# Optimization experiments

Measured on AMD Instinct MI355X. Metric: run time of the kernel, lower is better.

## Reference

```python
import jax, jax.numpy as jnp
import numpy as np

EPS = 1e-6
H, HKV, D = 32, 8, 64          # heads, kv heads, head_dim
E, TOP_K, FF = 8, 2, 1024      # experts, top-k, expert intermediate
HID = 2048


def rms_norm(x, w):
    xf = x.astype(jnp.float32)
    var = jnp.mean(xf * xf, axis=-1, keepdims=True)
    return (w * (xf * jax.lax.rsqrt(var + EPS)).astype(x.dtype))


def rotate_half(x):
    x1, x2 = jnp.split(x, 2, axis=-1)
    return jnp.concatenate([-x2, x1], axis=-1)


def apply_rope(q, k, cos, sin):
    # cos/sin: [B,S,rd] -> [B,1,S,rd]
    cos = cos[:, None, :, :]
    sin = sin[:, None, :, :]
    rd = cos.shape[-1]
    q_rot, q_pass = q[..., :rd], q[..., rd:]
    k_rot, k_pass = k[..., :rd], k[..., rd:]
    q_emb = q_rot * cos + rotate_half(q_rot) * sin
    k_emb = k_rot * cos + rotate_half(k_rot) * sin
    return (jnp.concatenate([q_emb, q_pass], -1), jnp.concatenate([k_emb, k_pass], -1))


def attention(x, cos, sin, wq, wk, wv, wo):
    B, S, _ = x.shape
    q = (x @ wq).reshape(B, S, H, D).transpose(0, 2, 1, 3)      # [B,H,S,D]
    k = (x @ wk).reshape(B, S, HKV, D).transpose(0, 2, 1, 3)    # [B,Hk,S,D]
    v = (x @ wv).reshape(B, S, HKV, D).transpose(0, 2, 1, 3)
    q, k = apply_rope(q, k, cos, sin)
    rep = H // HKV
    k = jnp.repeat(k, rep, axis=1)
    v = jnp.repeat(v, rep, axis=1)
    scale = D ** -0.5
    scores = jnp.einsum('bhqd,bhkd->bhqk', q, k) * scale
    causal = jnp.triu(jnp.full((S, S), -jnp.inf, dtype=scores.dtype), k=1)
    scores = scores + causal
    probs = jax.nn.softmax(scores.astype(jnp.float32), axis=-1).astype(q.dtype)
    out = jnp.einsum('bhqk,bhkd->bhqd', probs, v)
    out = out.transpose(0, 2, 1, 3).reshape(B, S, H * D)
    return out @ wo


def moe(x, gate_w, corr_bias, w1, w2, w3):
    B, S, Dm = x.shape
    xf = x.reshape(-1, Dm)                                      # [T, Dm]
    T = xf.shape[0]
    logits = xf @ gate_w                                        # [T, E]
    rw = jax.nn.sigmoid(logits.astype(jnp.float32))
    scores = rw + corr_bias
    _, sel = jax.lax.top_k(scores, TOP_K)                       # [T, k]
    tw = jnp.take_along_axis(rw, sel, axis=-1)
    tw = tw / jnp.sum(tw, axis=-1, keepdims=True)
    # dense [T, E] combine weights (zero for unselected experts)
    cw = jnp.zeros((T, E), dtype=xf.dtype).at[jnp.arange(T)[:, None], sel].set(tw.astype(xf.dtype))
    # run every expert densely, combine with sparse weights (same math as gather/scatter loop)
    h = jax.nn.silu(jnp.einsum('td,edf->etf', xf, w1)) * jnp.einsum('td,edf->etf', xf, w3)
    eo = jnp.einsum('etf,efd->etd', h, w2)                      # [E, T, Dm]
    out = jnp.einsum('etd,te->td', eo, cw)
    return out.reshape(B, S, Dm)


def setup_inputs() -> dict:
    key = jax.random.key(0)
    ks = jax.random.split(key, 16)
    s = 0.02
    return {
        'hidden_states': jax.random.normal(ks[0], (2, 1024, HID), jnp.float32),
        'cos': jax.random.uniform(ks[1], (2, 1024, D), jnp.float32),
        'sin': jax.random.uniform(ks[2], (2, 1024, D), jnp.float32),
        'ln1_w': jnp.ones((HID,), jnp.float32),
        'ln2_w': jnp.ones((HID,), jnp.float32),
        'wq': jax.random.normal(ks[3], (HID, H * D), jnp.float32) * s,
        'wk': jax.random.normal(ks[4], (HID, HKV * D), jnp.float32) * s,
        'wv': jax.random.normal(ks[5], (HID, HKV * D), jnp.float32) * s,
        'wo': jax.random.normal(ks[6], (H * D, HID), jnp.float32) * s,
        'gate_w': jax.random.normal(ks[7], (HID, E), jnp.float32) * s,
        'corr_bias': jnp.zeros((E,), jnp.float32),
        'w1': jax.random.normal(ks[8], (E, HID, FF), jnp.float32) * s,
        'w2': jax.random.normal(ks[9], (E, FF, HID), jnp.float32) * s,
        'w3': jax.random.normal(ks[10], (E, HID, FF), jnp.float32) * s,
    }


def reference(hidden_states, cos, sin, ln1_w, ln2_w, wq, wk, wv, wo, gate_w, corr_bias, w1, w2, w3):
    residual = hidden_states
    h = rms_norm(hidden_states, ln1_w)
    h = attention(h, cos, sin, wq, wk, wv, wo)
    h = residual + h
    residual = h
    h = rms_norm(h, ln2_w)
    h = moe(h, gate_w, corr_bias, w1, w2, w3)
    return residual + h
```

## Files before the change

### kernel.cpp

```cpp
#include <hip/hip_runtime.h>
#include <hip/hip_bf16.h>

#define DEV static __device__ __forceinline__

typedef __attribute__((ext_vector_type(8))) short short8;
typedef __attribute__((ext_vector_type(8))) __bf16 bf16x8;
typedef __attribute__((ext_vector_type(4))) float floatx4;

DEV short f2bf(float f) {
  unsigned u = __builtin_bit_cast(unsigned, f);
  unsigned r = (u + 0x7fffu + ((u >> 16) & 1u)) >> 16;
  return (short)(unsigned short)r;
}
DEV float bf2f(short s) {
  unsigned u = ((unsigned)(unsigned short)s) << 16;
  return __builtin_bit_cast(float, u);
}
DEV floatx4 mfma16(short8 a, short8 b, floatx4 c) {
  return __builtin_amdgcn_mfma_f32_16x16x32_bf16(
      __builtin_bit_cast(bf16x8, a), __builtin_bit_cast(bf16x8, b), c, 0, 0, 0);
}

#define VMCNT(n) asm volatile("s_waitcnt vmcnt(" #n ")" ::: "memory")
#define SBAR() __builtin_amdgcn_s_barrier()

DEV int sw2(int r) { return (r ^ (r >> 2)) & 3; }

DEV const short* sbase(const short* src, int ld, int row0, int id) {
  int r = id >> 2, cc = id & 3;
  return src + (long)(row0 + r) * ld + ((cc ^ sw2(r)) << 3);
}
DEV void sissue(short* ldsbuf, const short* base, int k0, int tid, int slotbase) {
  int wave = tid >> 6;
  __builtin_amdgcn_global_load_lds(
      (const __attribute__((address_space(1))) void*)(base + k0),
      (__attribute__((address_space(3))) void*)(ldsbuf + (slotbase + wave * 64) * 8),
      16, 0, 0);
}
DEV short8 rdfrag(const short* lds, int row, int l4) {
  return *(const short8*)(lds + row * 32 + ((l4 ^ sw2(row)) << 3));
}

DEV const short* sb64(const short* src, int ld, int row0, int id) {
  int r = id >> 3, c = id & 7;
  return src + (long)(row0 + r) * ld + ((c ^ (r & 7)) << 3);
}
DEV const short* sb64g(const short* src, int ld, const int* rows, int p0, int plim,
                       int id) {
  int r = id >> 3, c = id & 7;
  int pi = p0 + r;
  if (pi > plim) pi = plim;
  return src + (long)rows[pi] * ld + ((c ^ (r & 7)) << 3);
}
DEV short8 rd64(const short* lds, int row, int ch) {
  return *(const short8*)(lds + row * 64 + ((ch ^ (row & 7)) << 3));
}

__global__ __launch_bounds__(256) void k_gemm_qkv(
    const short* Ah, const short* Al, const short* Bh, const short* Bl,
    short* qbh, short* qbl, short* kbh, short* kbl, short* vbh, short* vbl,
    const float* cs, const float* sn) {
  const int K = 2048;
  __shared__ __align__(16) short AsH[2][4096], AsL[2][4096], BsH[2][4096], BsL[2][4096];
  int tid = threadIdx.x, lane = tid & 63, wave = tid >> 6;
  int l15 = lane & 15, l4 = lane >> 4;
  int wm = wave >> 1, wn = wave & 1;
  int bid = blockIdx.y * 24 + blockIdx.x;
  int swz = (bid & 7) * 48 + (bid >> 3);
  int bx = swz % 24, by = swz / 24;
  int m0 = by * 128, n0 = bx * 128;

  const short* bAH0 = sbase(Ah, K, m0, tid);
  const short* bAH1 = sbase(Ah, K, m0, tid + 256);
  const short* bAL0 = sbase(Al, K, m0, tid);
  const short* bAL1 = sbase(Al, K, m0, tid + 256);
  const short* bBH0 = sbase(Bh, K, n0, tid);
  const short* bBH1 = sbase(Bh, K, n0, tid + 256);
  const short* bBL0 = sbase(Bl, K, n0, tid);
  const short* bBL1 = sbase(Bl, K, n0, tid + 256);

  auto STAGE = [&](int buf, int k0) {
    sissue(AsH[buf], bAH0, k0, tid, 0);
    sissue(AsH[buf], bAH1, k0, tid, 256);
    sissue(AsL[buf], bAL0, k0, tid, 0);
    sissue(AsL[buf], bAL1, k0, tid, 256);
    sissue(BsH[buf], bBH0, k0, tid, 0);
    sissue(BsH[buf], bBH1, k0, tid, 256);
    sissue(BsL[buf], bBL0, k0, tid, 0);
    sissue(BsL[buf], bBL1, k0, tid, 256);
  };

  floatx4 zero4 = {0.f, 0.f, 0.f, 0.f};
  floatx4 acc[4][4];
#pragma unroll
  for (int i = 0; i < 4; ++i)
#pragma unroll
    for (int j = 0; j < 4; ++j) acc[i][j] = zero4;

  STAGE(0, 0);
  STAGE(1, 32);
  int cur = 0;
  for (int k0 = 0; k0 < K; k0 += 32) {
    if (k0 + 64 < K) VMCNT(8); else VMCNT(0);
    SBAR();
    short8 ah[4], al[4], bh2[4], bl2[4];
#pragma unroll
    for (int mi = 0; mi < 4; ++mi) {
      ah[mi] = rdfrag(AsH[cur], wm * 64 + mi * 16 + l15, l4);
      al[mi] = rdfrag(AsL[cur], wm * 64 + mi * 16 + l15, l4);
    }
#pragma unroll
    for (int nt = 0; nt < 4; ++nt) {
      bh2[nt] = rdfrag(BsH[cur], wn * 64 + nt * 16 + l15, l4);
      bl2[nt] = rdfrag(BsL[cur], wn * 64 + nt * 16 + l15, l4);
    }
#pragma unroll
    for (int mi = 0; mi < 4; ++mi)
#pragma unroll
      for (int nt = 0; nt < 4; ++nt) {
        acc[mi][nt] = mfma16(al[mi], bh2[nt], acc[mi][nt]);
        acc[mi][nt] = mfma16(ah[mi], bl2[nt], acc[mi][nt]);
        acc[mi][nt] = mfma16(ah[mi], bh2[nt], acc[mi][nt]);
      }
    SBAR();
    if (k0 + 64 < K) STAGE(cur, k0 + 64);
    cur ^= 1;
  }

  int hb = n0 + wn * 64;
  bool isq = hb < 2048, isk = (!isq) && hb < 2560;
  if (isq || isk) {
#pragma unroll
    for (int mi = 0; mi < 4; ++mi)
#pragma unroll
      for (int ntp = 0; ntp < 2; ++ntp)
#pragma unroll
        for (int j = 0; j < 4; ++j) {
          int row = m0 + wm * 64 + mi * 16 + l4 * 4 + j;
          int d = ntp * 16 + l15;
          float x0 = acc[mi][ntp][j], x1 = acc[mi][ntp + 2][j];
          float c0 = cs[row * 64 + d], c1 = cs[row * 64 + d + 32];
          float s0 = sn[row * 64 + d], s1 = sn[row * 64 + d + 32];
          float y0 = x0 * c0 - x1 * s0;
          float y1 = x1 * c1 + x0 * s1;
          if (isq) { y0 *= 0.125f; y1 *= 0.125f; }
          acc[mi][ntp][j] = y0;
          acc[mi][ntp + 2][j] = y1;
        }
  }
  short* Ch; short* Cl; int ldc, coff;
  if (isq)      { Ch = qbh; Cl = qbl; ldc = 2048; coff = hb; }
  else if (isk) { Ch = kbh; Cl = kbl; ldc = 512;  coff = hb - 2048; }
  else          { Ch = vbh; Cl = vbl; ldc = 512;  coff = hb - 2560; }
#pragma unroll
  for (int mi = 0; mi < 4; ++mi)
#pragma unroll
    for (int nt = 0; nt < 4; ++nt) {
      int row = m0 + wm * 64 + mi * 16 + l4 * 4;
      int col = coff + nt * 16 + l15;
#pragma unroll
      for (int j = 0; j < 4; ++j) {
        float v = acc[mi][nt][j];
        long ix = (long)(row + j) * ldc + col;
        short hi = f2bf(v);
        Ch[ix] = hi;
        Cl[ix] = f2bf(v - bf2f(hi));
      }
    }
}

__global__ __launch_bounds__(256) void k_gemm_wo(const short* Ah, const short* Al,
                                                 const short* Bh, const short* Bl,
                                                 const float* resid, float* out) {
  const int K = 2048;
  __shared__ __align__(16) short AsH[2][4096], AsL[2][4096], BsH[2][2048], BsL[2][2048];
  int tid = threadIdx.x, lane = tid & 63, wave = tid >> 6;
  int l15 = lane & 15, l4 = lane >> 4;
  int m0 = blockIdx.y * 128, n0 = blockIdx.x * 64;

  const short* bAH0 = sbase(Ah, K, m0, tid);
  const short* bAH1 = sbase(Ah, K, m0, tid + 256);
  const short* bAL0 = sbase(Al, K, m0, tid);
  const short* bAL1 = sbase(Al, K, m0, tid + 256);
  const short* bBH0 = sbase(Bh, K, n0, tid);
  const short* bBL0 = sbase(Bl, K, n0, tid);

  auto STAGE = [&](int buf, int k0) {
    sissue(AsH[buf], bAH0, k0, tid, 0);
    sissue(AsH[buf], bAH1, k0, tid, 256);
    sissue(AsL[buf], bAL0, k0, tid, 0);
    sissue(AsL[buf], bAL1, k0, tid, 256);
    sissue(BsH[buf], bBH0, k0, tid, 0);
    sissue(BsL[buf], bBL0, k0, tid, 0);
  };

  floatx4 zero4 = {0.f, 0.f, 0.f, 0.f};
  floatx4 acc[2][4];
#pragma unroll
  for (int i = 0; i < 2; ++i)
#pragma unroll
    for (int j = 0; j < 4; ++j) acc[i][j] = zero4;

  STAGE(0, 0);
  STAGE(1, 32);
  int cur = 0;
  for (int k0 = 0; k0 < K; k0 += 32) {
    if (k0 + 64 < K) VMCNT(6); else VMCNT(0);
    SBAR();
    short8 ah[2], al[2], bh2[4], bl2[4];
#pragma unroll
    for (int mi = 0; mi < 2; ++mi) {
      ah[mi] = rdfrag(AsH[cur], wave * 32 + mi * 16 + l15, l4);
      al[mi] = rdfrag(AsL[cur], wave * 32 + mi * 16 + l15, l4);
    }
#pragma unroll
    for (int nt = 0; nt < 4; ++nt) {
      bh2[nt] = rdfrag(BsH[cur], nt * 16 + l15, l4);
      bl2[nt] = rdfrag(BsL[cur], nt * 16 + l15, l4);
    }
#pragma unroll
    for (int mi = 0; mi < 2; ++mi)
#pragma unroll
      for (int nt = 0; nt < 4; ++nt) {
        acc[mi][nt] = mfma16(al[mi], bh2[nt], acc[mi][nt]);
        acc[mi][nt] = mfma16(ah[mi], bl2[nt], acc[mi][nt]);
        acc[mi][nt] = mfma16(ah[mi], bh2[nt], acc[mi][nt]);
      }
    SBAR();
    if (k0 + 64 < K) STAGE(cur, k0 + 64);
    cur ^= 1;
  }
#pragma unroll
  for (int mi = 0; mi < 2; ++mi)
#pragma unroll
    for (int nt = 0; nt < 4; ++nt) {
      int row = m0 + wave * 32 + mi * 16 + l4 * 4;
      int col = n0 + nt * 16 + l15;
#pragma unroll
      for (int j = 0; j < 4; ++j) {
        long ix = (long)(row + j) * 2048 + col;
        out[ix] = resid[ix] + acc[mi][nt][j];
      }
    }
}

__global__ __launch_bounds__(256) void k_moe_a(const short* X, const short* W1T,
                                               const short* W3T, const int* rows,
                                               const int* cnt, const int* eoff,
                                               short* hh) {
  int e = blockIdx.z;
  int c = cnt[e];
  int mtile = blockIdx.y;
  if (mtile * 128 >= c) return;
  int p0 = eoff[e] + mtile * 128;
  int plim = eoff[e] + c - 1;
  const short* B1 = W1T + (long)e * 1024 * 2048;
  const short* B3 = W3T + (long)e * 1024 * 2048;
  int n0 = blockIdx.x * 64;
  __shared__ __align__(16) short As_[2][8192], B1s[2][4096], B3s[2][4096];
  int tid = threadIdx.x, lane = tid & 63, wave = tid >> 6;
  int l15 = lane & 15, l4 = lane >> 4;
  int wm = wave >> 1, wn = wave & 1;

  const short* bA0 = sb64g(X, 2048, rows, p0, plim, tid);
  const short* bA1 = sb64g(X, 2048, rows, p0, plim, tid + 256);
  const short* bA2 = sb64g(X, 2048, rows, p0, plim, tid + 512);
  const short* bA3 = sb64g(X, 2048, rows, p0, plim, tid + 768);
  const short* bB1_0 = sb64(B1, 2048, n0, tid);
  const short* bB1_1 = sb64(B1, 2048, n0, tid + 256);
  const short* bB3_0 = sb64(B3, 2048, n0, tid);
  const short* bB3_1 = sb64(B3, 2048, n0, tid + 256);

  auto STAGE = [&](int buf, int k0) {
    sissue(As_[buf], bA0, k0, tid, 0);
    sissue(As_[buf], bA1, k0, tid, 256);
    sissue(As_[buf], bA2, k0, tid, 512);
    sissue(As_[buf], bA3, k0, tid, 768);
    sissue(B1s[buf], bB1_0, k0, tid, 0);
    sissue(B1s[buf], bB1_1, k0, tid, 256);
    sissue(B3s[buf], bB3_0, k0, tid, 0);
    sissue(B3s[buf], bB3_1, k0, tid, 256);
  };

  floatx4 zero4 = {0.f, 0.f, 0.f, 0.f};
  floatx4 acc1[4][2], acc3[4][2];
#pragma unroll
  for (int i = 0; i < 4; ++i)
#pragma unroll
    for (int j = 0; j < 2; ++j) { acc1[i][j] = zero4; acc3[i][j] = zero4; }

  STAGE(0, 0);
  STAGE(1, 64);
  int cur = 0;
  for (int k0 = 0; k0 < 2048; k0 += 64) {
    if (k0 + 128 < 2048) VMCNT(8); else VMCNT(0);
    SBAR();
#pragma unroll
    for (int kh = 0; kh < 2; ++kh) {
      int ch = kh * 4 + l4;
      short8 af[4], b1f[2], b3f[2];
#pragma unroll
      for (int mi = 0; mi < 4; ++mi)
        af[mi] = rd64(As_[cur], wm * 64 + mi * 16 + l15, ch);
#pragma unroll
      for (int nt = 0; nt < 2; ++nt) {
        b1f[nt] = rd64(B1s[cur], wn * 32 + nt * 16 + l15, ch);
        b3f[nt] = rd64(B3s[cur], wn * 32 + nt * 16 + l15, ch);
      }
#pragma unroll
      for (int mi = 0; mi < 4; ++mi)
#pragma unroll
        for (int nt = 0; nt < 2; ++nt) {
          acc1[mi][nt] = mfma16(af[mi], b1f[nt], acc1[mi][nt]);
          acc3[mi][nt] = mfma16(af[mi], b3f[nt], acc3[mi][nt]);
        }
    }
    SBAR();
    if (k0 + 128 < 2048) STAGE(cur, k0 + 128);
    cur ^= 1;
  }
#pragma unroll
  for (int mi = 0; mi < 4; ++mi)
#pragma unroll
    for (int nt = 0; nt < 2; ++nt) {
      int col = n0 + wn * 32 + nt * 16 + l15;
#pragma unroll
      for (int j = 0; j < 4; ++j) {
        int rl = wm * 64 + mi * 16 + l4 * 4 + j;
        if (mtile * 128 + rl < c) {
          float v1 = acc1[mi][nt][j], v3 = acc3[mi][nt][j];
          float hg = v1 / (1.f + __expf(-v1));
          hh[(long)(p0 + rl) * 1024 + col] = f2bf(hg * v3);
        }
      }
    }
}

__global__ __launch_bounds__(256) void k_moe_b(const short* hh, const short* W2T,
                                               const int* cnt, const int* eoff,
                                               short* mo) {
  int e = blockIdx.z;
  int c = cnt[e];
  int mtile = blockIdx.y;
  if (mtile * 128 >= c) return;
  int p0 = eoff[e] + mtile * 128;
  const short* B = W2T + (long)e * 2048 * 1024;
  int n0 = blockIdx.x * 128;
  __shared__ __align__(16) short As_[2][8192], Bs_[2][8192];
  int tid = threadIdx.x, lane = tid & 63, wave = tid >> 6;
  int l15 = lane & 15, l4 = lane >> 4;
  int wm = wave >> 1, wn = wave & 1;

  const short* bA0 = sb64(hh, 1024, p0, tid);
  const short* bA1 = sb64(hh, 1024, p0, tid + 256);
  const short* bA2 = sb64(hh, 1024, p0, tid + 512);
  const short* bA3 = sb64(hh, 1024, p0, tid + 768);
  const short* bB0 = sb64(B, 1024, n0, tid);
  const short* bB1 = sb64(B, 1024, n0, tid + 256);
  const short* bB2 = sb64(B, 1024, n0, tid + 512);
  const short* bB3 = sb64(B, 1024, n0, tid + 768);

  auto STAGE = [&](int buf, int k0) {
    sissue(As_[buf], bA0, k0, tid, 0);
    sissue(As_[buf], bA1, k0, tid, 256);
    sissue(As_[buf], bA2, k0, tid, 512);
    sissue(As_[buf], bA3, k0, tid, 768);
    sissue(Bs_[buf], bB0, k0, tid, 0);
    sissue(Bs_[buf], bB1, k0, tid, 256);
    sissue(Bs_[buf], bB2, k0, tid, 512);
    sissue(Bs_[buf], bB3, k0, tid, 768);
  };

  floatx4 zero4 = {0.f, 0.f, 0.f, 0.f};
  floatx4 acc[4][4];
#pragma unroll
  for (int i = 0; i < 4; ++i)
#pragma unroll
    for (int j = 0; j < 4; ++j) acc[i][j] = zero4;

  STAGE(0, 0);
  STAGE(1, 64);
  int cur = 0;
  for (int k0 = 0; k0 < 1024; k0 += 64) {
    if (k0 + 128 < 1024) VMCNT(8); else VMCNT(0);
    SBAR();
#pragma unroll
    for (int kh = 0; kh < 2; ++kh) {
      int ch = kh * 4 + l4;
      short8 af[4], bfv[4];
#pragma unroll
      for (int mi = 0; mi < 4; ++mi)
        af[mi] = rd64(As_[cur], wm * 64 + mi * 16 + l15, ch);
#pragma unroll
      for (int nt = 0; nt < 4; ++nt)
        bfv[nt] = rd64(Bs_[cur], wn * 64 + nt * 16 + l15, ch);
#pragma unroll
      for (int mi = 0; mi < 4; ++mi)
#pragma unroll
        for (int nt = 0; nt < 4; ++nt)
          acc[mi][nt] = mfma16(af[mi], bfv[nt], acc[mi][nt]);
    }
    SBAR();
    if (k0 + 128 < 1024) STAGE(cur, k0 + 128);
    cur ^= 1;
  }
#pragma unroll
  for (int mi = 0; mi < 4; ++mi)
#pragma unroll
    for (int nt = 0; nt < 4; ++nt) {
      int col = n0 + wn * 64 + nt * 16 + l15;
#pragma unroll
      for (int j = 0; j < 4; ++j) {
        int rl = wm * 64 + mi * 16 + l4 * 4 + j;
        if (mtile * 128 + rl < c) mo[(long)(p0 + rl) * 2048 + col] = f2bf(acc[mi][nt][j]);
      }
    }
}

__global__ __launch_bounds__(256) void k_transv(const short* vbh, const short* vbl,
                                                short* vth, short* vtl) {
  __shared__ __align__(16) short th[64][72], tl[64][72];
  int tt = blockIdx.x;
  int bk = blockIdx.y;
  int b = bk >> 3, kvh = bk & 7;
  int tid = threadIdx.x;
#pragma unroll
  for (int it = 0; it < 2; ++it) {
    int id = it * 256 + tid;
    int r = id >> 3, cc = id & 7;
    long src = (long)(b * 1024 + tt * 64 + r) * 512 + kvh * 64 + cc * 8;
    *(uint4*)(&th[r][cc * 8]) = *(const uint4*)(vbh + src);
    *(uint4*)(&tl[r][cc * 8]) = *(const uint4*)(vbl + src);
  }
  __syncthreads();
#pragma unroll
  for (int it = 0; it < 2; ++it) {
    int id = it * 256 + tid;
    int n = id >> 3, kc = id & 7;
    short8 oh2, ol2;
#pragma unroll
    for (int j = 0; j < 8; ++j) { oh2[j] = th[kc * 8 + j][n]; ol2[j] = tl[kc * 8 + j][n]; }
    long dst = (long)bk * 65536 + (long)n * 1024 + tt * 64 + kc * 8;
    *(short8*)(vth + dst) = oh2;
    *(short8*)(vtl + dst) = ol2;
  }
}

DEV int vsw(int r) { return (r ^ (r >> 3)) & 7; }
DEV short8 avread(const short* buf, int row, int c) {
  return *(const short8*)(buf + row * 64 + (((c ^ vsw(row)) & 7) << 3));
}
DEV int aswz(int r, int c) { return r * 64 + (((c ^ ((r ^ (r >> 3)) & 7)) & 7) << 3); }
DEV void glds(short* ldsslot, const short* src) {
  __builtin_amdgcn_global_load_lds(
      (const __attribute__((address_space(1))) void*)src,
      (__attribute__((address_space(3))) void*)ldsslot, 16, 0, 0);
}

__global__ __launch_bounds__(256) void k_attn3(
    const short* qhp, const short* qlp, const short* khp, const short* klp,
    const short* vth2, const short* vtl2, short* oh, short* ol) {
  int xp = blockIdx.x, bh = blockIdx.y;
  int h = bh & 31, b = bh >> 5, kvh = h >> 2;
  int tid = threadIdx.x, wave = tid >> 6, lane = tid & 63;
  int l15 = lane & 15, l4 = lane >> 4;
  int qtA = 15 - xp, qtB = xp;

  __shared__ __align__(16) short Kh[2][4096], Kl[2][4096], Vh[2][4096], Vl[2][4096];
  __shared__ __align__(16) short Ph[4][1024], Pl[4][1024];

  short8 qh[2][2], ql[2][2];
#pragma unroll
  for (int tt = 0; tt < 2; ++tt) {
    int qrow = (tt ? qtB : qtA) * 64 + wave * 16 + l15;
    long qoff = ((long)(b * 1024 + qrow)) * 2048 + h * 64;
    qh[tt][0] = *(const short8*)(qhp + qoff + l4 * 8);
    qh[tt][1] = *(const short8*)(qhp + qoff + 32 + l4 * 8);
    ql[tt][0] = *(const short8*)(qlp + qoff + l4 * 8);
    ql[tt][1] = *(const short8*)(qlp + qoff + 32 + l4 * 8);
  }

  floatx4 zero4 = {0.f, 0.f, 0.f, 0.f};
  floatx4 acco[2][4];
  float mrun[2][4], lrun[2][4];
#pragma unroll
  for (int tt = 0; tt < 2; ++tt)
#pragma unroll
    for (int j = 0; j < 4; ++j) {
      acco[tt][j] = zero4;
      mrun[tt][j] = -1e30f;
      lrun[tt][j] = 0.f;
    }

  const short* khb = khp + ((long)b * 1024) * 512 + kvh * 64;
  const short* klb = klp + ((long)b * 1024) * 512 + kvh * 64;
  const short* vhb = vth2 + (long)(b * 8 + kvh) * 65536;
  const short* vlb = vtl2 + (long)(b * 8 + kvh) * 65536;

  int r0 = tid >> 3, c0 = tid & 7;
  int r1 = r0 + 32;
  const short* kh0 = khb + (long)r0 * 512 + ((c0 ^ vsw(r0)) << 3);
  const short* kh1 = khb + (long)r1 * 512 + ((c0 ^ vsw(r1)) << 3);
  const short* kl0 = klb + (long)r0 * 512 + ((c0 ^ vsw(r0)) << 3);
  const short* kl1 = klb + (long)r1 * 512 + ((c0 ^ vsw(r1)) << 3);
  const short* vh0 = vhb + (long)r0 * 1024 + ((c0 ^ vsw(r0)) << 3);
  const short* vh1 = vhb + (long)r1 * 1024 + ((c0 ^ vsw(r1)) << 3);
  const short* vl0 = vlb + (long)r0 * 1024 + ((c0 ^ vsw(r0)) << 3);
  const short* vl1 = vlb + (long)r1 * 1024 + ((c0 ^ vsw(r1)) << 3);
  int wslot = wave * 512;

  auto STAGE = [&](int buf, int kt) {
    int ko = kt * 32768;
    int vo = kt * 64;
    glds(&Kh[buf][wslot], kh0 + ko);
    glds(&Kh[buf][2048 + wslot], kh1 + ko);
    glds(&Kl[buf][wslot], kl0 + ko);
    glds(&Kl[buf][2048 + wslot], kl1 + ko);
    glds(&Vh[buf][wslot], vh0 + vo);
    glds(&Vh[buf][2048 + wslot], vh1 + vo);
    glds(&Vl[buf][wslot], vl0 + vo);
    glds(&Vl[buf][2048 + wslot], vl1 + vo);
  };

  STAGE(0, 0);
  int cur = 0;
  for (int kt = 0; kt <= qtA; ++kt) {
    __syncthreads();
    if (kt < qtA) STAGE(cur ^ 1, kt + 1);
#pragma unroll
    for (int tt = 0; tt < 2; ++tt) {
      int qtt = tt ? qtB : qtA;
      if (tt == 1 && kt > qtB) continue;
      floatx4 accs[4] = {zero4, zero4, zero4, zero4};
#pragma unroll
      for (int ks = 0; ks < 2; ++ks) {
        short8 qah = qh[tt][ks];
        short8 qal = ql[tt][ks];
#pragma unroll
        for (int nt = 0; nt < 4; ++nt) {
          int kvr = nt * 16 + l15;
          short8 kfh = avread(Kh[cur], kvr, l4 + 4 * ks);
          short8 kfl = avread(Kl[cur], kvr, l4 + 4 * ks);
          accs[nt] = mfma16(qal, kfh, accs[nt]);
          accs[nt] = mfma16(qah, kfl, accs[nt]);
          accs[nt] = mfma16(qah, kfh, accs[nt]);
        }
      }
      if (kt == qtt) {
#pragma unroll
        for (int nt = 0; nt < 4; ++nt)
#pragma unroll
          for (int j = 0; j < 4; ++j) {
            int kvg = nt * 16 + l15;
            int qg = wave * 16 + l4 * 4 + j;
            if (kvg > qg) accs[nt][j] = -1e30f;
          }
      }
      float pj[4][4];
#pragma unroll
      for (int j = 0; j < 4; ++j) {
        float mx = fmaxf(fmaxf(accs[0][j], accs[1][j]), fmaxf(accs[2][j], accs[3][j]));
        mx = fmaxf(mx, __shfl_xor(mx, 1));
        mx = fmaxf(mx, __shfl_xor(mx, 2));
        mx = fmaxf(mx, __shfl_xor(mx, 4));
        mx = fmaxf(mx, __shfl_xor(mx, 8));
        float mnew = fmaxf(mrun[tt][j], mx);
        float alpha = __expf(mrun[tt][j] - mnew);
        float rs = 0.f;
#pragma unroll
        for (int nt = 0; nt < 4; ++nt) {
          float pv = __expf(accs[nt][j] - mnew);
          pj[nt][j] = pv;
          rs += pv;
        }
        rs += __shfl_xor(rs, 1);
        rs += __shfl_xor(rs, 2);
        rs += __shfl_xor(rs, 4);
        rs += __shfl_xor(rs, 8);
        lrun[tt][j] = lrun[tt][j] * alpha + rs;
        mrun[tt][j] = mnew;
        acco[tt][0][j] *= alpha; acco[tt][1][j] *= alpha;
        acco[tt][2][j] *= alpha; acco[tt][3][j] *= alpha;
      }
      short* P = Ph[wave];
      short* P2 = Pl[wave];
#pragma unroll
      for (int nt = 0; nt < 4; ++nt)
#pragma unroll
        for (int j = 0; j < 4; ++j) {
          int rr = l4 * 4 + j, col = nt * 16 + l15;
          float pv = pj[nt][j];
          short hi = f2bf(pv);
          int ad = aswz(rr, col >> 3) + (col & 7);
          P[ad] = hi;
          P2[ad] = f2bf(pv - bf2f(hi));
        }
      asm volatile("s_waitcnt lgkmcnt(0)" ::: "memory");
      __builtin_amdgcn_sched_barrier(0);
#pragma unroll
      for (int ks = 0; ks < 2; ++ks) {
        short8 pah = *(const short8*)(P + aswz(l15, l4 + 4 * ks));
        short8 pal = *(const short8*)(P2 + aswz(l15, l4 + 4 * ks));
#pragma unroll
        for (int nt = 0; nt < 4; ++nt) {
          int dr = nt * 16 + l15;
          short8 vfh = avread(Vh[cur], dr, l4 + 4 * ks);
          short8 vfl = avread(Vl[cur], dr, l4 + 4 * ks);
          acco[tt][nt] = mfma16(pal, vfh, acco[tt][nt]);
          acco[tt][nt] = mfma16(pah, vfl, acco[tt][nt]);
          acco[tt][nt] = mfma16(pah, vfh, acco[tt][nt]);
        }
      }
    }
    cur ^= 1;
  }
#pragma unroll
  for (int tt = 0; tt < 2; ++tt) {
    int qtt = tt ? qtB : qtA;
#pragma unroll
    for (int j = 0; j < 4; ++j) {
      float invl = 1.f / lrun[tt][j];
      int qg = qtt * 64 + wave * 16 + l4 * 4 + j;
      long ooff = ((long)(b * 1024 + qg)) * 2048 + h * 64;
#pragma unroll
      for (int nt = 0; nt < 4; ++nt) {
        float v = acco[tt][nt][j] * invl;
        short hi = f2bf(v);
        oh[ooff + nt * 16 + l15] = hi;
        ol[ooff + nt * 16 + l15] = f2bf(v - bf2f(hi));
      }
    }
  }
}

DEV void trans_load(const float* src, int N, int n0, int k0, float (*t)[65], int tid) {
  int r = tid >> 2, cq = tid & 3;
  const float* s = src + (long)(k0 + r) * N + n0 + cq * 16;
#pragma unroll
  for (int i = 0; i < 4; ++i) {
    float4 v = *(const float4*)(s + i * 4);
    t[r][cq * 16 + i * 4 + 0] = v.x;
    t[r][cq * 16 + i * 4 + 1] = v.y;
    t[r][cq * 16 + i * 4 + 2] = v.z;
    t[r][cq * 16 + i * 4 + 3] = v.w;
  }
}

DEV void trans_tile1(const float* src, short* dst, int N, int K, int n0, int k0,
                     float (*t)[65]) {
  int tid = threadIdx.x;
  trans_load(src, N, n0, k0, t, tid);
  __syncthreads();
  int n = tid >> 2, kc = tid & 3;
#pragma unroll
  for (int ii = 0; ii < 2; ++ii) {
    short8 o;
#pragma unroll
    for (int j = 0; j < 8; ++j) o[j] = f2bf(t[kc * 16 + ii * 8 + j][n]);
    *(short8*)(dst + (long)(n0 + n) * K + k0 + kc * 16 + ii * 8) = o;
  }
}

DEV void trans_tile2(const float* src, short* dh, short* dl, int N, int K, int n0,
                     int k0, float (*t)[65]) {
  int tid = threadIdx.x;
  trans_load(src, N, n0, k0, t, tid);
  __syncthreads();
  int n = tid >> 2, kc = tid & 3;
#pragma unroll
  for (int ii = 0; ii < 2; ++ii) {
    short8 ohv, olv;
#pragma unroll
    for (int j = 0; j < 8; ++j) {
      float v = t[kc * 16 + ii * 8 + j][n];
      short hi = f2bf(v);
      ohv[j] = hi;
      olv[j] = f2bf(v - bf2f(hi));
    }
    *(short8*)(dh + (long)(n0 + n) * K + k0 + kc * 16 + ii * 8) = ohv;
    *(short8*)(dl + (long)(n0 + n) * K + k0 + kc * 16 + ii * 8) = olv;
  }
}

__global__ __launch_bounds__(256) void k_trans_attn(
    const float* wq, const float* wk, const float* wv, const float* wo,
    short* qkvTh, short* qkvTl, short* woTh, short* woTl) {
  __shared__ float t[64][65];
  int x = blockIdx.x, kt = blockIdx.y;
  const float* src; short* dh; short* dl; int N, n0;
  if (x < 32)      { src = wq; dh = qkvTh; dl = qkvTl; N = 2048; n0 = x * 64; }
  else if (x < 40) { src = wk; dh = qkvTh + 2048L * 2048; dl = qkvTl + 2048L * 2048;
                     N = 512; n0 = (x - 32) * 64; }
  else if (x < 48) { src = wv; dh = qkvTh + 2560L * 2048; dl = qkvTl + 2560L * 2048;
                     N = 512; n0 = (x - 40) * 64; }
  else             { src = wo; dh = woTh; dl = woTl; N = 2048; n0 = (x - 48) * 64; }
  trans_tile2(src, dh, dl, N, 2048, n0, kt * 64, t);
}

__global__ __launch_bounds__(256) void k_trans_moe13(const float* w1, const float* w3,
                                                     short* w1T, short* w3T) {
  __shared__ float t[64][65];
  int x = blockIdx.x, kt = blockIdx.y;
  const float* src; short* dst; int n0;
  if (x < 128) { int e = x >> 4; src = w1 + (long)e * 2048 * 1024;
                 dst = w1T + (long)e * 1024 * 2048; n0 = (x & 15) * 64; }
  else         { int i = x - 128, e = i >> 4; src = w3 + (long)e * 2048 * 1024;
                 dst = w3T + (long)e * 1024 * 2048; n0 = (i & 15) * 64; }
  trans_tile1(src, dst, 1024, 2048, n0, kt * 64, t);
}

__global__ __launch_bounds__(256) void k_trans_w2(const float* w2, short* w2T) {
  __shared__ float t[64][65];
  int e = blockIdx.x >> 5, ntb = blockIdx.x & 31, kt = blockIdx.y;
  trans_tile1(w2 + (long)e * 1024 * 2048, w2T + (long)e * 2048 * 1024,
              2048, 1024, ntb * 64, kt * 64, t);
}

__global__ __launch_bounds__(256) void k_rmsnorm1(const float* x, const float* w,
                                                  short* outh, short* outl) {
  int row = blockIdx.x, tid = threadIdx.x;
  const float* xr = x + (long)row * 2048;
  float4 a = *(const float4*)(xr + tid * 8);
  float4 c = *(const float4*)(xr + tid * 8 + 4);
  float ss = a.x * a.x + a.y * a.y + a.z * a.z + a.w * a.w +
             c.x * c.x + c.y * c.y + c.z * c.z + c.w * c.w;
  ss += __shfl_xor(ss, 1);  ss += __shfl_xor(ss, 2);  ss += __shfl_xor(ss, 4);
  ss += __shfl_xor(ss, 8);  ss += __shfl_xor(ss, 16); ss += __shfl_xor(ss, 32);
  __shared__ float red[4];
  int wave = tid >> 6;
  if ((tid & 63) == 0) red[wave] = ss;
  __syncthreads();
  float tot = red[0] + red[1] + red[2] + red[3];
  float inv = 1.f / sqrtf(tot * (1.f / 2048.f) + 1e-6f);
  float4 w0 = *(const float4*)(w + tid * 8);
  float4 w1 = *(const float4*)(w + tid * 8 + 4);
  float xv[8] = {a.x * w0.x, a.y * w0.y, a.z * w0.z, a.w * w0.w,
                 c.x * w1.x, c.y * w1.y, c.z * w1.z, c.w * w1.w};
  short8 ohv, olv;
#pragma unroll
  for (int j = 0; j < 8; ++j) {
    float v = xv[j] * inv;
    short hi = f2bf(v);
    ohv[j] = hi;
    olv[j] = f2bf(v - bf2f(hi));
  }
  *(short8*)(outh + (long)row * 2048 + tid * 8) = ohv;
  *(short8*)(outl + (long)row * 2048 + tid * 8) = olv;
}

__global__ __launch_bounds__(256) void k_rmsnorm2_gate(const float* x, const float* w,
                                                       const float* gw, const float* cb,
                                                       short* out, int* sel, float* tw,
                                                       int* cnt) {
  int row = blockIdx.x, tid = threadIdx.x;
  const float* xr = x + (long)row * 2048;
  float4 a = *(const float4*)(xr + tid * 8);
  float4 c = *(const float4*)(xr + tid * 8 + 4);
  float ss = a.x * a.x + a.y * a.y + a.z * a.z + a.w * a.w +
             c.x * c.x + c.y * c.y + c.z * c.z + c.w * c.w;
  ss += __shfl_xor(ss, 1);  ss += __shfl_xor(ss, 2);  ss += __shfl_xor(ss, 4);
  ss += __shfl_xor(ss, 8);  ss += __shfl_xor(ss, 16); ss += __shfl_xor(ss, 32);
  __shared__ float red[4];
  int wave = tid >> 6;
  if ((tid & 63) == 0) red[wave] = ss;
  __syncthreads();
  float tot = red[0] + red[1] + red[2] + red[3];
  float inv = 1.f / sqrtf(tot * (1.f / 2048.f) + 1e-6f);
  float4 w0 = *(const float4*)(w + tid * 8);
  float4 w1 = *(const float4*)(w + tid * 8 + 4);
  float xn[8];
  xn[0] = a.x * inv * w0.x; xn[1] = a.y * inv * w0.y; xn[2] = a.z * inv * w0.z;
  xn[3] = a.w * inv * w0.w; xn[4] = c.x * inv * w1.x; xn[5] = c.y * inv * w1.y;
  xn[6] = c.z * inv * w1.z; xn[7] = c.w * inv * w1.w;
  short8 o;
#pragma unroll
  for (int j = 0; j < 8; ++j) o[j] = f2bf(xn[j]);
  *(short8*)(out + (long)row * 2048 + tid * 8) = o;
  float gp[8] = {0.f, 0.f, 0.f, 0.f, 0.f, 0.f, 0.f, 0.f};
#pragma unroll
  for (int j = 0; j < 8; ++j) {
    const float* g = gw + (long)(tid * 8 + j) * 8;
    float4 g0 = *(const float4*)g;
    float4 g1 = *(const float4*)(g + 4);
    gp[0] += xn[j] * g0.x; gp[1] += xn[j] * g0.y; gp[2] += xn[j] * g0.z; gp[3] += xn[j] * g0.w;
    gp[4] += xn[j] * g1.x; gp[5] += xn[j] * g1.y; gp[6] += xn[j] * g1.z; gp[7] += xn[j] * g1.w;
  }
#pragma unroll
  for (int e = 0; e < 8; ++e) {
    gp[e] += __shfl_xor(gp[e], 1);  gp[e] += __shfl_xor(gp[e], 2);
    gp[e] += __shfl_xor(gp[e], 4);  gp[e] += __shfl_xor(gp[e], 8);
    gp[e] += __shfl_xor(gp[e], 16); gp[e] += __shfl_xor(gp[e], 32);
  }
  __shared__ float gred[4][8];
  __shared__ float srw[8], ssc[8];
  if ((tid & 63) == 0) {
#pragma unroll
    for (int e = 0; e < 8; ++e) gred[wave][e] = gp[e];
  }
  __syncthreads();
  if (tid < 8) {
    float lg = gred[0][tid] + gred[1][tid] + gred[2][tid] + gred[3][tid];
    float rw = 1.f / (1.f + expf(-lg));
    srw[tid] = rw;
    ssc[tid] = rw + cb[tid];
  }
  __syncthreads();
  if (tid == 0) {
    int e0 = 0; float b0 = ssc[0];
    for (int e = 1; e < 8; ++e) if (ssc[e] > b0) { b0 = ssc[e]; e0 = e; }
    int e1 = -1; float b1 = -1e30f;
    for (int e = 0; e < 8; ++e) if (e != e0 && ssc[e] > b1) { b1 = ssc[e]; e1 = e; }
    float t0 = srw[e0], t1 = srw[e1], s = t0 + t1;
    sel[row * 2] = e0; sel[row * 2 + 1] = e1;
    tw[row * 2] = t0 / s; tw[row * 2 + 1] = t1 / s;
    atomicAdd(&cnt[e0], 1);
    atomicAdd(&cnt[e1], 1);
  }
}

__global__ void k_scan(const int* cnt, int* eoff) {
  if (threadIdx.x == 0) {
    int s = 0;
    for (int e = 0; e < 8; ++e) { eoff[e] = s; s += cnt[e]; }
  }
}

__global__ __launch_bounds__(256) void k_scatter(const int* sel, const int* eoff,
                                                 int* fill, int* rows, int* pos) {
  int t = blockIdx.x * 256 + threadIdx.x;
  if (t >= 2048) return;
  for (int k = 0; k < 2; ++k) {
    int e = sel[t * 2 + k];
    int p = eoff[e] + atomicAdd(&fill[e], 1);
    rows[p] = t;
    pos[t * 2 + k] = p;
  }
}

__global__ __launch_bounds__(256) void k_combine(float* out, const short* mo,
                                                 const int* pos, const float* tw) {
  int t = blockIdx.x, tid = threadIdx.x;
  int p0 = pos[t * 2], p1 = pos[t * 2 + 1];
  float w0 = tw[t * 2], w1 = tw[t * 2 + 1];
  float* o = out + (long)t * 2048 + tid * 8;
  short8 m0 = *(const short8*)(mo + (long)p0 * 2048 + tid * 8);
  short8 m1 = *(const short8*)(mo + (long)p1 * 2048 + tid * 8);
  float4 a = *(const float4*)o;
  float4 b = *(const float4*)(o + 4);
  a.x += w0 * bf2f(m0[0]) + w1 * bf2f(m1[0]);
  a.y += w0 * bf2f(m0[1]) + w1 * bf2f(m1[1]);
  a.z += w0 * bf2f(m0[2]) + w1 * bf2f(m1[2]);
  a.w += w0 * bf2f(m0[3]) + w1 * bf2f(m1[3]);
  b.x += w0 * bf2f(m0[4]) + w1 * bf2f(m1[4]);
  b.y += w0 * bf2f(m0[5]) + w1 * bf2f(m1[5]);
  b.z += w0 * bf2f(m0[6]) + w1 * bf2f(m1[6]);
  b.w += w0 * bf2f(m0[7]) + w1 * bf2f(m1[7]);
  *(float4*)o = a;
  *(float4*)(o + 4) = b;
}

extern "C" void kernel_launch(void* const* d_in, const int* in_sizes, int n_in,
                              void* d_out, int out_size, void* d_ws, size_t ws_size,
                              hipStream_t stream) {
  const float* x    = (const float*)d_in[0];
  const float* cosb = (const float*)d_in[1];
  const float* sinb = (const float*)d_in[2];
  const float* ln1  = (const float*)d_in[3];
  const float* ln2  = (const float*)d_in[4];
  const float* wq   = (const float*)d_in[5];
  const float* wk   = (const float*)d_in[6];
  const float* wv   = (const float*)d_in[7];
  const float* wo   = (const float*)d_in[8];
  const float* gw   = (const float*)d_in[9];
  const float* cb   = (const float*)d_in[10];
  const float* w1   = (const float*)d_in[11];
  const float* w2   = (const float*)d_in[12];
  const float* w3   = (const float*)d_in[13];
  float* out = (float*)d_out;

  char* p = (char*)d_ws;
  auto take = [&](size_t n) { char* r = p; p += (n + 255) & ~(size_t)255; return r; };
  short* qkvTh = (short*)take(3072L * 2048 * 2);
  short* qkvTl = (short*)take(3072L * 2048 * 2);
  short* woTh  = (short*)take(2048L * 2048 * 2);
  short* woTl  = (short*)take(2048L * 2048 * 2);
  short* w1T   = (short*)take(8L * 1024 * 2048 * 2);
  short* w3T   = (short*)take(8L * 1024 * 2048 * 2);
  short* w2T   = (short*)take(8L * 2048 * 1024 * 2);
  short* hbh   = (short*)take(2048L * 2048 * 2);
  short* hbl   = (short*)take(2048L * 2048 * 2);
  short* qbh   = (short*)take(2048L * 2048 * 2);
  short* qbl   = (short*)take(2048L * 2048 * 2);
  short* kbh   = (short*)take(2048L * 512 * 2);
  short* kbl   = (short*)take(2048L * 512 * 2);
  short* vbh   = (short*)take(2048L * 512 * 2);
  short* vbl   = (short*)take(2048L * 512 * 2);
  short* vth   = (short*)take(16L * 64 * 1024 * 2);
  short* vtl   = (short*)take(16L * 64 * 1024 * 2);
  short* aoh   = (short*)take(2048L * 2048 * 2);
  short* aol   = (short*)take(2048L * 2048 * 2);
  short* h2b   = (short*)take(2048L * 2048 * 2);
  short* hhb   = (short*)take(4224L * 1024 * 2);
  short* mob   = (short*)take(4352L * 2048 * 2);
  int* rti     = (int*)take(64 * sizeof(int));
  int* cnt = rti; int* fill = rti + 8; int* eoff = rti + 16;
  int* sel     = (int*)take(2048L * 2 * 4);
  float* twb   = (float*)take(2048L * 2 * 4);
  int* rowsp   = (int*)take(4352L * 4);
  int* posb    = (int*)take(2048L * 2 * 4);
  (void)ws_size; (void)in_sizes; (void)n_in; (void)out_size;

  dim3 B256(256);
  k_trans_attn<<<dim3(80, 32), B256, 0, stream>>>(wq, wk, wv, wo, qkvTh, qkvTl,
                                                  woTh, woTl);
  k_trans_moe13<<<dim3(256, 32), B256, 0, stream>>>(w1, w3, w1T, w3T);
  k_trans_w2<<<dim3(256, 16), B256, 0, stream>>>(w2, w2T);
  hipMemsetAsync(rti, 0, 64, stream);

  k_rmsnorm1<<<dim3(2048), B256, 0, stream>>>(x, ln1, hbh, hbl);
  k_gemm_qkv<<<dim3(24, 16), B256, 0, stream>>>(hbh, hbl, qkvTh, qkvTl, qbh, qbl,
                                                kbh, kbl, vbh, vbl, cosb, sinb);
  k_transv<<<dim3(16, 16), B256, 0, stream>>>(vbh, vbl, vth, vtl);
  k_attn3<<<dim3(8, 64), B256, 0, stream>>>(qbh, qbl, kbh, kbl, vth, vtl, aoh, aol);
  k_gemm_wo<<<dim3(32, 16), B256, 0, stream>>>(aoh, aol, woTh, woTl, x, out);

  k_rmsnorm2_gate<<<dim3(2048), B256, 0, stream>>>(out, ln2, gw, cb, h2b, sel, twb, cnt);
  k_scan<<<dim3(1), dim3(64), 0, stream>>>(cnt, eoff);
  k_scatter<<<dim3(8), B256, 0, stream>>>(sel, eoff, fill, rowsp, posb);
  k_moe_a<<<dim3(16, 16, 8), B256, 0, stream>>>(h2b, w1T, w3T, rowsp, cnt, eoff, hhb);
  k_moe_b<<<dim3(16, 16, 8), B256, 0, stream>>>(hhb, w2T, cnt, eoff, mob);
  k_combine<<<dim3(2048), B256, 0, stream>>>(out, mob, posb, twb);
}
```

Baseline: 550.9 us.

## Pre-pack attention weights in MFMA fragment order and load B directly to registers

The weight transpose kernel for Wq/Wk/Wv/Wo now writes hi/lo bf16 splits in a packed per-64-column-panel layout that matches the MFMA B-fragment lane order. The QKV and output-projection GEMMs then read B fragments straight from global memory into registers with coalesced 16-byte loads, skipping LDS staging for B. This cuts LDS traffic and footprint, which may raise occupancy. In exchange, the B loads are no longer prefetched ahead and their latency is exposed inside each k-step, guarded only by a vmcnt wait.

```diff
diff --git a/kernel.cpp b/kernel.cpp
--- a/kernel.cpp
+++ b/kernel.cpp
@@ -57,11 +57,11 @@
 }
 
 __global__ __launch_bounds__(256) void k_gemm_qkv(
-    const short* Ah, const short* Al, const short* Bh, const short* Bl,
+    const short* Ah, const short* Al, const short* BpH, const short* BpL,
     short* qbh, short* qbl, short* kbh, short* kbl, short* vbh, short* vbl,
     const float* cs, const float* sn) {
   const int K = 2048;
-  __shared__ __align__(16) short AsH[2][4096], AsL[2][4096], BsH[2][4096], BsL[2][4096];
+  __shared__ __align__(16) short AsH[2][4096], AsL[2][4096];
   int tid = threadIdx.x, lane = tid & 63, wave = tid >> 6;
   int l15 = lane & 15, l4 = lane >> 4;
   int wm = wave >> 1, wn = wave & 1;
@@ -69,25 +69,20 @@
   int swz = (bid & 7) * 48 + (bid >> 3);
   int bx = swz % 24, by = swz / 24;
   int m0 = by * 128, n0 = bx * 128;
+  int p = (n0 >> 6) + wn;
 
   const short* bAH0 = sbase(Ah, K, m0, tid);
   const short* bAH1 = sbase(Ah, K, m0, tid + 256);
   const short* bAL0 = sbase(Al, K, m0, tid);
   const short* bAL1 = sbase(Al, K, m0, tid + 256);
-  const short* bBH0 = sbase(Bh, K, n0, tid);
-  const short* bBH1 = sbase(Bh, K, n0, tid + 256);
-  const short* bBL0 = sbase(Bl, K, n0, tid);
-  const short* bBL1 = sbase(Bl, K, n0, tid + 256);
-
-  auto STAGE = [&](int buf, int k0) {
+  const short* bph = BpH + (long)p * 131072 + lane * 8;
+  const short* bpl = BpL + (long)p * 131072 + lane * 8;
+
+  auto STAGEA = [&](int buf, int k0) {
     sissue(AsH[buf], bAH0, k0, tid, 0);
     sissue(AsH[buf], bAH1, k0, tid, 256);
     sissue(AsL[buf], bAL0, k0, tid, 0);
     sissue(AsL[buf], bAL1, k0, tid, 256);
-    sissue(BsH[buf], bBH0, k0, tid, 0);
-    sissue(BsH[buf], bBH1, k0, tid, 256);
-    sissue(BsL[buf], bBL0, k0, tid, 0);
-    sissue(BsL[buf], bBL1, k0, tid, 256);
   };
 
   floatx4 zero4 = {0.f, 0.f, 0.f, 0.f};
@@ -97,22 +92,24 @@
 #pragma unroll
     for (int j = 0; j < 4; ++j) acc[i][j] = zero4;
 
-  STAGE(0, 0);
-  STAGE(1, 32);
+  STAGEA(0, 0);
+  STAGEA(1, 32);
   int cur = 0;
   for (int k0 = 0; k0 < K; k0 += 32) {
-    if (k0 + 64 < K) VMCNT(8); else VMCNT(0);
+    int ks = k0 >> 5;
     SBAR();
-    short8 ah[4], al[4], bh2[4], bl2[4];
+    short8 bh2[4], bl2[4];
+#pragma unroll
+    for (int nt = 0; nt < 4; ++nt) {
+      bh2[nt] = *(const short8*)(bph + (ks * 4 + nt) * 512);
+      bl2[nt] = *(const short8*)(bpl + (ks * 4 + nt) * 512);
+    }
+    VMCNT(8);
+    short8 ah[4], al[4];
 #pragma unroll
     for (int mi = 0; mi < 4; ++mi) {
       ah[mi] = rdfrag(AsH[cur], wm * 64 + mi * 16 + l15, l4);
       al[mi] = rdfrag(AsL[cur], wm * 64 + mi * 16 + l15, l4);
-    }
-#pragma unroll
-    for (int nt = 0; nt < 4; ++nt) {
-      bh2[nt] = rdfrag(BsH[cur], wn * 64 + nt * 16 + l15, l4);
-      bl2[nt] = rdfrag(BsL[cur], wn * 64 + nt * 16 + l15, l4);
     }
 #pragma unroll
     for (int mi = 0; mi < 4; ++mi)
@@ -123,12 +120,11 @@
         acc[mi][nt] = mfma16(ah[mi], bh2[nt], acc[mi][nt]);
       }
     SBAR();
-    if (k0 + 64 < K) STAGE(cur, k0 + 64);
+    if (k0 + 64 < K) STAGEA(cur, k0 + 64);
     cur ^= 1;
   }
 
-  int hb = n0 + wn * 64;
-  bool isq = hb < 2048, isk = (!isq) && hb < 2560;
+  bool isq = p < 32, isk = (!isq) && p < 40;
   if (isq || isk) {
 #pragma unroll
     for (int mi = 0; mi < 4; ++mi)
@@ -149,9 +145,9 @@
         }
   }
   short* Ch; short* Cl; int ldc, coff;
-  if (isq)      { Ch = qbh; Cl = qbl; ldc = 2048; coff = hb; }
-  else if (isk) { Ch = kbh; Cl = kbl; ldc = 512;  coff = hb - 2048; }
-  else          { Ch = vbh; Cl = vbl; ldc = 512;  coff = hb - 2560; }
+  if (isq)      { Ch = qbh; Cl = qbl; ldc = 2048; coff = p * 64; }
+  else if (isk) { Ch = kbh; Cl = kbl; ldc = 512;  coff = (p - 32) * 64; }
+  else          { Ch = vbh; Cl = vbl; ldc = 512;  coff = (p - 40) * 64; }
 #pragma unroll
   for (int mi = 0; mi < 4; ++mi)
 #pragma unroll
@@ -170,28 +166,27 @@
 }
 
 __global__ __launch_bounds__(256) void k_gemm_wo(const short* Ah, const short* Al,
-                                                 const short* Bh, const short* Bl,
+                                                 const short* BpH, const short* BpL,
                                                  const float* resid, float* out) {
   const int K = 2048;
-  __shared__ __align__(16) short AsH[2][4096], AsL[2][4096], BsH[2][2048], BsL[2][2048];
+  __shared__ __align__(16) short AsH[2][4096], AsL[2][4096];
   int tid = threadIdx.x, lane = tid & 63, wave = tid >> 6;
   int l15 = lane & 15, l4 = lane >> 4;
   int m0 = blockIdx.y * 128, n0 = blockIdx.x * 64;
+  int p = n0 >> 6;
 
   const short* bAH0 = sbase(Ah, K, m0, tid);
   const short* bAH1 = sbase(Ah, K, m0, tid + 256);
   const short* bAL0 = sbase(Al, K, m0, tid);
   const short* bAL1 = sbase(Al, K, m0, tid + 256);
-  const short* bBH0 = sbase(Bh, K, n0, tid);
-  const short* bBL0 = sbase(Bl, K, n0, tid);
-
-  auto STAGE = [&](int buf, int k0) {
+  const short* bph = BpH + (long)p * 131072 + lane * 8;
+  const short* bpl = BpL + (long)p * 131072 + lane * 8;
+
+  auto STAGEA = [&](int buf, int k0) {
     sissue(AsH[buf], bAH0, k0, tid, 0);
     sissue(AsH[buf], bAH1, k0, tid, 256);
     sissue(AsL[buf], bAL0, k0, tid, 0);
     sissue(AsL[buf], bAL1, k0, tid, 256);
-    sissue(BsH[buf], bBH0, k0, tid, 0);
-    sissue(BsL[buf], bBL0, k0, tid, 0);
   };
 
   floatx4 zero4 = {0.f, 0.f, 0.f, 0.f};
@@ -201,22 +196,24 @@
 #pragma unroll
     for (int j = 0; j < 4; ++j) acc[i][j] = zero4;
 
-  STAGE(0, 0);
-  STAGE(1, 32);
+  STAGEA(0, 0);
+  STAGEA(1, 32);
   int cur = 0;
   for (int k0 = 0; k0 < K; k0 += 32) {
-    if (k0 + 64 < K) VMCNT(6); else VMCNT(0);
+    int ks = k0 >> 5;
     SBAR();
-    short8 ah[2], al[2], bh2[4], bl2[4];
+    short8 bh2[4], bl2[4];
+#pragma unroll
+    for (int nt = 0; nt < 4; ++nt) {
+      bh2[nt] = *(const short8*)(bph + (ks * 4 + nt) * 512);
+      bl2[nt] = *(const short8*)(bpl + (ks * 4 + nt) * 512);
+    }
+    VMCNT(8);
+    short8 ah[2], al[2];
 #pragma unroll
     for (int mi = 0; mi < 2; ++mi) {
       ah[mi] = rdfrag(AsH[cur], wave * 32 + mi * 16 + l15, l4);
       al[mi] = rdfrag(AsL[cur], wave * 32 + mi * 16 + l15, l4);
-    }
-#pragma unroll
-    for (int nt = 0; nt < 4; ++nt) {
-      bh2[nt] = rdfrag(BsH[cur], nt * 16 + l15, l4);
-      bl2[nt] = rdfrag(BsL[cur], nt * 16 + l15, l4);
     }
 #pragma unroll
     for (int mi = 0; mi < 2; ++mi)
@@ -227,7 +224,7 @@
         acc[mi][nt] = mfma16(ah[mi], bh2[nt], acc[mi][nt]);
       }
     SBAR();
-    if (k0 + 64 < K) STAGE(cur, k0 + 64);
+    if (k0 + 64 < K) STAGEA(cur, k0 + 64);
     cur ^= 1;
   }
 #pragma unroll
@@ -661,40 +658,43 @@
   }
 }
 
-DEV void trans_tile2(const float* src, short* dh, short* dl, int N, int K, int n0,
-                     int k0, float (*t)[65]) {
+DEV void trans_tile2p(const float* src, short* dph, short* dpl, int N, int n0,
+                      int k0, float (*t)[65]) {
   int tid = threadIdx.x;
   trans_load(src, N, n0, k0, t, tid);
   __syncthreads();
-  int n = tid >> 2, kc = tid & 3;
-#pragma unroll
-  for (int ii = 0; ii < 2; ++ii) {
-    short8 ohv, olv;
+  int wv = tid >> 6, lane = tid & 63;
+#pragma unroll
+  for (int it = 0; it < 2; ++it) {
+    int u = it * 4 + wv;
+    int ksl = u >> 2, nt = u & 3;
+    int kb = ksl * 32 + (lane >> 4) * 8;
+    int n = nt * 16 + (lane & 15);
+    short8 hv, lv;
 #pragma unroll
     for (int j = 0; j < 8; ++j) {
-      float v = t[kc * 16 + ii * 8 + j][n];
+      float v = t[kb + j][n];
       short hi = f2bf(v);
-      ohv[j] = hi;
-      olv[j] = f2bf(v - bf2f(hi));
-    }
-    *(short8*)(dh + (long)(n0 + n) * K + k0 + kc * 16 + ii * 8) = ohv;
-    *(short8*)(dl + (long)(n0 + n) * K + k0 + kc * 16 + ii * 8) = olv;
+      hv[j] = hi;
+      lv[j] = f2bf(v - bf2f(hi));
+    }
+    long off = ((long)((k0 >> 5) + ksl) * 4 + nt) * 512 + lane * 8;
+    *(short8*)(dph + off) = hv;
+    *(short8*)(dpl + off) = lv;
   }
 }
 
 __global__ __launch_bounds__(256) void k_trans_attn(
     const float* wq, const float* wk, const float* wv, const float* wo,
-    short* qkvTh, short* qkvTl, short* woTh, short* woTl) {
+    short* qkvPh, short* qkvPl, short* woPh, short* woPl) {
   __shared__ float t[64][65];
   int x = blockIdx.x, kt = blockIdx.y;
-  const float* src; short* dh; short* dl; int N, n0;
-  if (x < 32)      { src = wq; dh = qkvTh; dl = qkvTl; N = 2048; n0 = x * 64; }
-  else if (x < 40) { src = wk; dh = qkvTh + 2048L * 2048; dl = qkvTl + 2048L * 2048;
-                     N = 512; n0 = (x - 32) * 64; }
-  else if (x < 48) { src = wv; dh = qkvTh + 2560L * 2048; dl = qkvTl + 2560L * 2048;
-                     N = 512; n0 = (x - 40) * 64; }
-  else             { src = wo; dh = woTh; dl = woTl; N = 2048; n0 = (x - 48) * 64; }
-  trans_tile2(src, dh, dl, N, 2048, n0, kt * 64, t);
+  const float* src; short* dh; short* dl; int N, n0, pg;
+  if (x < 32)      { src = wq; N = 2048; n0 = x * 64; pg = x; dh = qkvPh; dl = qkvPl; }
+  else if (x < 40) { src = wk; N = 512; n0 = (x - 32) * 64; pg = x; dh = qkvPh; dl = qkvPl; }
+  else if (x < 48) { src = wv; N = 512; n0 = (x - 40) * 64; pg = x; dh = qkvPh; dl = qkvPl; }
+  else             { src = wo; N = 2048; n0 = (x - 48) * 64; pg = x - 48; dh = woPh; dl = woPl; }
+  trans_tile2p(src, dh + (long)pg * 131072, dl + (long)pg * 131072, N, n0, kt * 64, t);
 }
 
 __global__ __launch_bounds__(256) void k_trans_moe13(const float* w1, const float* w3,
@@ -880,10 +880,10 @@
 
   char* p = (char*)d_ws;
   auto take = [&](size_t n) { char* r = p; p += (n + 255) & ~(size_t)255; return r; };
-  short* qkvTh = (short*)take(3072L * 2048 * 2);
-  short* qkvTl = (short*)take(3072L * 2048 * 2);
-  short* woTh  = (short*)take(2048L * 2048 * 2);
-  short* woTl  = (short*)take(2048L * 2048 * 2);
+  short* qkvPh = (short*)take(3072L * 2048 * 2);
+  short* qkvPl = (short*)take(3072L * 2048 * 2);
+  short* woPh  = (short*)take(2048L * 2048 * 2);
+  short* woPl  = (short*)take(2048L * 2048 * 2);
   short* w1T   = (short*)take(8L * 1024 * 2048 * 2);
   short* w3T   = (short*)take(8L * 1024 * 2048 * 2);
   short* w2T   = (short*)take(8L * 2048 * 1024 * 2);
@@ -911,18 +911,18 @@
   (void)ws_size; (void)in_sizes; (void)n_in; (void)out_size;
 
   dim3 B256(256);
-  k_trans_attn<<<dim3(80, 32), B256, 0, stream>>>(wq, wk, wv, wo, qkvTh, qkvTl,
-                                                  woTh, woTl);
+  k_trans_attn<<<dim3(80, 32), B256, 0, stream>>>(wq, wk, wv, wo, qkvPh, qkvPl,
+                                                  woPh, woPl);
   k_trans_moe13<<<dim3(256, 32), B256, 0, stream>>>(w1, w3, w1T, w3T);
   k_trans_w2<<<dim3(256, 16), B256, 0, stream>>>(w2, w2T);
   hipMemsetAsync(rti, 0, 64, stream);
 
   k_rmsnorm1<<<dim3(2048), B256, 0, stream>>>(x, ln1, hbh, hbl);
-  k_gemm_qkv<<<dim3(24, 16), B256, 0, stream>>>(hbh, hbl, qkvTh, qkvTl, qbh, qbl,
+  k_gemm_qkv<<<dim3(24, 16), B256, 0, stream>>>(hbh, hbl, qkvPh, qkvPl, qbh, qbl,
                                                 kbh, kbl, vbh, vbl, cosb, sinb);
   k_transv<<<dim3(16, 16), B256, 0, stream>>>(vbh, vbl, vth, vtl);
   k_attn3<<<dim3(8, 64), B256, 0, stream>>>(qbh, qbl, kbh, kbl, vth, vtl, aoh, aol);
-  k_gemm_wo<<<dim3(32, 16), B256, 0, stream>>>(aoh, aol, woTh, woTl, x, out);
+  k_gemm_wo<<<dim3(32, 16), B256, 0, stream>>>(aoh, aol, woPh, woPl, x, out);
 
   k_rmsnorm2_gate<<<dim3(2048), B256, 0, stream>>>(out, ln2, gw, cb, h2b, sel, twb, cnt);
   k_scan<<<dim3(1), dim3(64), 0, stream>>>(cnt, eoff);
```

After: 575.1 us. +4.4%, slower.
